# Optimization experiments

Hardware: AMD Instinct MI355X
Metric: run time of the kernel (lower is better)

## Reference

```python
import jax, jax.numpy as jnp
import numpy as np

N = 100_000      # nodes
E = 1_600_000    # edges (avg degree 16)
IN, H, OUT = 960, 192, 3
NB = 6           # block_num


def setup_inputs() -> dict:
    key = jax.random.key(0)
    ks = jax.random.split(key, 14)
    s = 0.05  # weight init scale
    x = jax.random.normal(ks[0], (N, IN), jnp.float32)
    src = jax.random.randint(ks[1], (E,), 0, N, jnp.int32)
    dst = jax.random.randint(ks[2], (E,), 0, N, jnp.int32)
    # normalized adjacency values (like D^-1 A entries)
    ew = jax.random.uniform(ks[3], (E,), jnp.float32) / 16.0
    w1 = jax.random.normal(ks[4], (IN, H), jnp.float32) * s
    l1 = jax.random.normal(ks[5], (IN, H), jnp.float32) * s
    b1 = jnp.zeros((H,), jnp.float32)
    wb = jax.random.normal(ks[6], (2 * NB, H, H), jnp.float32) * s
    lb = jax.random.normal(ks[7], (2 * NB, H, H), jnp.float32) * s
    bb = jnp.zeros((2 * NB, H), jnp.float32)
    w2 = jax.random.normal(ks[8], (H, OUT), jnp.float32) * s
    l2 = jax.random.normal(ks[9], (H, OUT), jnp.float32) * s
    b2 = jnp.zeros((OUT,), jnp.float32)
    return dict(x=x, src=src, dst=dst, ew=ew, w1=w1, l1=l1, b1=b1,
                wb=wb, lb=lb, bb=bb, w2=w2, l2=l2, b2=b2)


def reference(x, src, dst, ew, w1, l1, b1, wb, lb, bb, w2, l2, b2):
    def gcn(h, w, lw, b):
        # GraphConvolution: spmm(adj, h @ w) + h @ loop_w + b
        sup = h @ w                                   # [N, F_out]
        msg = sup[src] * ew[:, None]                  # gather + weight  [E, F_out]
        agg = jax.ops.segment_sum(msg, dst, num_segments=N)
        return agg + h @ lw + b

    h = gcn(x, w1, l1, b1)                            # conv1: in_dim -> hidden
    for i in range(NB):                               # GResBlocks
        a = gcn(h, wb[2 * i], lb[2 * i], bb[2 * i])
        a = gcn(a, wb[2 * i + 1], lb[2 * i + 1], bb[2 * i + 1])
        h = (h + a) * 0.5                             # residual scaling
    x_cat = h
    x_out = gcn(x_cat, w2, l2, b2)                    # conv2: hidden -> out_dim
    return (x_out, x_cat)
```

## Files before the change

kernel.cpp:

```cpp
#include <hip/hip_runtime.h>

typedef __attribute__((ext_vector_type(8))) short short8;
typedef __attribute__((ext_vector_type(4))) float f32x4;
typedef __attribute__((ext_vector_type(4))) int int4v;
typedef __attribute__((ext_vector_type(2))) unsigned int u32x2;

__device__ __forceinline__ float bf2f(unsigned short u) {
  return __uint_as_float(((unsigned)u) << 16);
}
__device__ __forceinline__ unsigned short f2bf(float f) {
  unsigned u = __float_as_uint(f);
  return (unsigned short)((u + 0x7FFFu + ((u >> 16) & 1u)) >> 16);
}

#define GLB_CAST(p) ((const __attribute__((address_space(1))) void*)(p))
#define LDS_CAST(p) ((__attribute__((address_space(3))) void*)(p))

__global__ void count_kernel(const int* __restrict__ dst, int* __restrict__ cnt, int E) {
  int e = blockIdx.x * blockDim.x + threadIdx.x;
  if (e < E) atomicAdd(&cnt[dst[e] + 1], 1);
}

__global__ __launch_bounds__(256) void scan_bsum_kernel(const int* __restrict__ cnt,
                                                        int* __restrict__ bsum, int n) {
  __shared__ int buf[256];
  int tid = threadIdx.x;
  int j0 = blockIdx.x * 1024 + tid * 4;
  int s = 0;
#pragma unroll
  for (int k = 0; k < 4; k++) {
    int j = j0 + k;
    if (j < n) s += cnt[j];
  }
  buf[tid] = s;
  __syncthreads();
  for (int off = 128; off > 0; off >>= 1) {
    if (tid < off) buf[tid] += buf[tid + off];
    __syncthreads();
  }
  if (tid == 0) bsum[blockIdx.x] = buf[0];
}

__global__ __launch_bounds__(256) void scan_small_kernel(const int* __restrict__ bsum,
                                                         int* __restrict__ boff, int nb) {
  __shared__ int buf[2][256];
  int tid = threadIdx.x;
  int C = (nb + 255) >> 8;
  int start = tid * C;
  int end = start + C; if (end > nb) end = nb;
  int s = 0;
  for (int j = start; j < end; j++) s += bsum[j];
  buf[0][tid] = s;
  __syncthreads();
  int pin = 0;
  for (int off = 1; off < 256; off <<= 1) {
    int v = buf[pin][tid];
    if (tid >= off) v += buf[pin][tid - off];
    buf[pin ^ 1][tid] = v;
    pin ^= 1;
    __syncthreads();
  }
  int run = (tid == 0) ? 0 : buf[pin][tid - 1];
  for (int j = start; j < end; j++) {
    boff[j] = run;
    run += bsum[j];
  }
}

__global__ __launch_bounds__(256) void scan_final_kernel(const int* __restrict__ cnt,
                                                         const int* __restrict__ boff,
                                                         int* __restrict__ rowptr,
                                                         int* __restrict__ cur,
                                                         int n, int nrows) {
  __shared__ int buf[2][256];
  int tid = threadIdx.x;
  int j0 = blockIdx.x * 1024 + tid * 4;
  int v[4];
  int s = 0;
#pragma unroll
  for (int k = 0; k < 4; k++) {
    int j = j0 + k;
    v[k] = (j < n) ? cnt[j] : 0;
    s += v[k];
  }
  buf[0][tid] = s;
  __syncthreads();
  int pin = 0;
  for (int off = 1; off < 256; off <<= 1) {
    int t = buf[pin][tid];
    if (tid >= off) t += buf[pin][tid - off];
    buf[pin ^ 1][tid] = t;
    pin ^= 1;
    __syncthreads();
  }
  int run = boff[blockIdx.x] + ((tid == 0) ? 0 : buf[pin][tid - 1]);
#pragma unroll
  for (int k = 0; k < 4; k++) {
    int j = j0 + k;
    if (j < n) {
      run += v[k];
      rowptr[j] = run;
      if (j < nrows) cur[j] = run;
    }
  }
}

__global__ void fill_kernel(const int* __restrict__ src, const int* __restrict__ dst,
                            const float* __restrict__ ew,
                            int* __restrict__ cur, int2* __restrict__ s_edge, int E) {
  int e = blockIdx.x * blockDim.x + threadIdx.x;
  if (e >= E) return;
  int r = dst[e];
  int pos = atomicAdd(&cur[r], 1);
  s_edge[pos] = make_int2(src[e], __float_as_int(ew[e]));
}

__global__ void prep_w_kernel(const float* __restrict__ w1,
                              const float* __restrict__ l1,
                              const float* __restrict__ wb,
                              const float* __restrict__ lb,
                              unsigned short* __restrict__ Wt1,
                              unsigned short* __restrict__ Wtb) {
  int tid = blockIdx.x * blockDim.x + threadIdx.x;
  const int n1 = 384 * 960;
  const int nb = 12 * 384 * 192;
  if (tid < n1) {
    int c = tid / 960, k = tid % 960;
    Wt1[tid] = f2bf((c < 192) ? w1[k * 192 + c] : l1[k * 192 + (c - 192)]);
  } else if (tid < n1 + nb) {
    int u = tid - n1;
    int i = u / (384 * 192);
    int r = u % (384 * 192);
    int c = r / 192, k = r % 192;
    Wtb[u] = f2bf((c < 192) ? wb[(i * 192 + k) * 192 + c]
                            : lb[(i * 192 + k) * 192 + (c - 192)]);
  }
}

__device__ __forceinline__ short8 cvt_pair(f32x4 a, f32x4 b) {
  short8 r;
  r[0] = (short)f2bf(a[0]); r[1] = (short)f2bf(a[1]);
  r[2] = (short)f2bf(a[2]); r[3] = (short)f2bf(a[3]);
  r[4] = (short)f2bf(b[0]); r[5] = (short)f2bf(b[1]);
  r[6] = (short)f2bf(b[2]); r[7] = (short)f2bf(b[3]);
  return r;
}

__global__ __launch_bounds__(512) void gemm_f32_kernel(const float* __restrict__ A,
                                                       const unsigned short* __restrict__ Wt,
                                                       unsigned short* __restrict__ out,
                                                       int nrows, int K) {
  __shared__ char lds_raw[40960];

  int tid = threadIdx.x;
  int lane = tid & 63;
  int w = tid >> 6;
  int rg = w >> 1, ch = w & 1;
  int row0blk = blockIdx.x * 256;
  int row0 = row0blk + rg * 64;
  int l15 = lane & 15, lq = lane >> 4;

  f32x4 acc[12][4];
#pragma unroll
  for (int cf = 0; cf < 12; cf++)
#pragma unroll
    for (int rf = 0; rf < 4; rf++) acc[cf][rf] = (f32x4)(0.0f);

  int tiles = K / 32;
  for (int tile = 0; tile < tiles; ++tile) {
    __syncthreads();
#pragma unroll
    for (int it = 0; it < 3; ++it) {
      int slot = it * 512 + tid;
      int q = slot / 384, c = slot - q * 384;
      const unsigned short* g = Wt + (size_t)c * K + tile * 32 + q * 8;
      __builtin_amdgcn_global_load_lds(GLB_CAST(g), LDS_CAST(lds_raw + 16384 + slot * 16), 16, 0, 0);
    }
#pragma unroll
    for (int it = 0; it < 2; ++it) {
      int slot = it * 512 + tid;
      int c = slot >> 8, row = slot & 255;
      int grow = row0blk + row;
      if (grow > nrows - 1) grow = nrows - 1;
      const float* g = A + (size_t)grow * K + tile * 32 + c * 8;
      f32x4 a0 = *reinterpret_cast<const f32x4*>(g);
      f32x4 a1 = *reinterpret_cast<const f32x4*>(g + 4);
      *reinterpret_cast<short8*>(lds_raw + slot * 16) = cvt_pair(a0, a1);
    }
    __syncthreads();

    short8 af[4];
#pragma unroll
    for (int rf = 0; rf < 4; rf++)
      af[rf] = *reinterpret_cast<const short8*>(
          lds_raw + lq * 4096 + (rg * 64 + rf * 16 + l15) * 16);
#pragma unroll
    for (int cf = 0; cf < 12; cf++) {
      const short8 bf = *reinterpret_cast<const short8*>(
          lds_raw + 16384 + (lq * 384 + ch * 192 + cf * 16 + l15) * 16);
#pragma unroll
      for (int rf = 0; rf < 4; rf++)
        acc[cf][rf] = __builtin_amdgcn_mfma_f32_16x16x32_bf16(bf, af[rf], acc[cf][rf], 0, 0, 0);
    }
  }

#pragma unroll
  for (int rf = 0; rf < 4; rf++) {
    int row = row0 + rf * 16 + l15;
    if (row >= nrows) continue;
    unsigned short* orow = out + (size_t)row * 384 + ch * 192 + lq * 4;
#pragma unroll
    for (int cf = 0; cf < 12; cf++) {
      u32x2 pv;
      pv[0] = (unsigned)f2bf(acc[cf][rf][0]) | ((unsigned)f2bf(acc[cf][rf][1]) << 16);
      pv[1] = (unsigned)f2bf(acc[cf][rf][2]) | ((unsigned)f2bf(acc[cf][rf][3]) << 16);
      *reinterpret_cast<u32x2*>(orow + cf * 16) = pv;
    }
  }
}

__global__ __launch_bounds__(512) void gemm_bf16_db_kernel(const unsigned short* __restrict__ A,
                                                           const unsigned short* __restrict__ Wt,
                                                           unsigned short* __restrict__ out,
                                                           int nrows, int K) {
  extern __shared__ char lds_db[];

  int tid = threadIdx.x;
  int lane = tid & 63;
  int w = tid >> 6;
  int rg = w >> 1, ch = w & 1;
  int row0blk = blockIdx.x * 256;
  int row0 = row0blk + rg * 64;
  int l15 = lane & 15, lq = lane >> 4;

  f32x4 acc[12][4];
#pragma unroll
  for (int cf = 0; cf < 12; cf++)
#pragma unroll
    for (int rf = 0; rf < 4; rf++) acc[cf][rf] = (f32x4)(0.0f);

  auto stage = [&](int tile, int buf) {
    char* base = lds_db + buf * 40960;
#pragma unroll
    for (int it = 0; it < 3; ++it) {
      int slot = it * 512 + tid;
      int q = slot / 384, c = slot - q * 384;
      const unsigned short* g = Wt + (size_t)c * K + tile * 32 + q * 8;
      __builtin_amdgcn_global_load_lds(GLB_CAST(g), LDS_CAST(base + 16384 + slot * 16), 16, 0, 0);
    }
#pragma unroll
    for (int it = 0; it < 2; ++it) {
      int slot = it * 512 + tid;
      int c = slot >> 8, row = slot & 255;
      int grow = row0blk + row;
      if (grow > nrows - 1) grow = nrows - 1;
      const unsigned short* g = A + (size_t)grow * K + tile * 32 + c * 8;
      __builtin_amdgcn_global_load_lds(GLB_CAST(g), LDS_CAST(base + slot * 16), 16, 0, 0);
    }
  };

  int tiles = K / 32;
  stage(0, 0);
  __syncthreads();
  int cur = 0;
  for (int tile = 0; tile < tiles; ++tile) {
    if (tile + 1 < tiles) stage(tile + 1, cur ^ 1);
    char* base = lds_db + cur * 40960;
    short8 af[4];
#pragma unroll
    for (int rf = 0; rf < 4; rf++)
      af[rf] = *reinterpret_cast<const short8*>(
          base + lq * 4096 + (rg * 64 + rf * 16 + l15) * 16);
#pragma unroll
    for (int cf = 0; cf < 12; cf++) {
      const short8 bf = *reinterpret_cast<const short8*>(
          base + 16384 + (lq * 384 + ch * 192 + cf * 16 + l15) * 16);
#pragma unroll
      for (int rf = 0; rf < 4; rf++)
        acc[cf][rf] = __builtin_amdgcn_mfma_f32_16x16x32_bf16(bf, af[rf], acc[cf][rf], 0, 0, 0);
    }
    __syncthreads();
    cur ^= 1;
  }

#pragma unroll
  for (int rf = 0; rf < 4; rf++) {
    int row = row0 + rf * 16 + l15;
    if (row >= nrows) continue;
    unsigned short* orow = out + (size_t)row * 384 + ch * 192 + lq * 4;
#pragma unroll
    for (int cf = 0; cf < 12; cf++) {
      u32x2 pv;
      pv[0] = (unsigned)f2bf(acc[cf][rf][0]) | ((unsigned)f2bf(acc[cf][rf][1]) << 16);
      pv[1] = (unsigned)f2bf(acc[cf][rf][2]) | ((unsigned)f2bf(acc[cf][rf][3]) << 16);
      *reinterpret_cast<u32x2*>(orow + cf * 16) = pv;
    }
  }
}

__global__ __launch_bounds__(256) void spmm_kernel(const unsigned short* __restrict__ t,
                                                   const int* __restrict__ rowptr,
                                                   const int2* __restrict__ s_edge,
                                                   const float* __restrict__ bias,
                                                   const unsigned short* __restrict__ hprev16,
                                                   unsigned short* __restrict__ out16,
                                                   int n, int mode) {
  int tid = blockIdx.x * blockDim.x + threadIdx.x;
  int node = tid >> 3;
  int sub = tid & 7;
  if (node >= n) return;
  int co = sub * 8;

  float acc[3][8];
#pragma unroll
  for (int q = 0; q < 3; q++)
#pragma unroll
    for (int j = 0; j < 8; j++) acc[q][j] = 0.0f;

  int e0 = rowptr[node], e1 = rowptr[node + 1];
  int ne = e1 - e0;
  int base = 0;
  for (; base + 8 <= ne; base += 8) {
    int2 rec = s_edge[e0 + base + sub];
#pragma unroll
    for (int half = 0; half < 2; half++) {
      short8 v[4][3];
      float wgt[4];
#pragma unroll
      for (int k = 0; k < 4; k++) {
        int kk = half * 4 + k;
        int sn = __shfl(rec.x, kk, 8);
        wgt[k] = __int_as_float(__shfl(rec.y, kk, 8));
        const unsigned short* row = t + (size_t)sn * 384;
#pragma unroll
        for (int q = 0; q < 3; q++)
          v[k][q] = *reinterpret_cast<const short8*>(row + q * 64 + co);
      }
#pragma unroll
      for (int k = 0; k < 4; k++)
#pragma unroll
        for (int q = 0; q < 3; q++)
#pragma unroll
          for (int j = 0; j < 8; j++)
            acc[q][j] += wgt[k] * bf2f((unsigned short)v[k][q][j]);
    }
  }
  for (; base < ne; base++) {
    int2 rec = s_edge[e0 + base];
    float wgt = __int_as_float(rec.y);
    const unsigned short* row = t + (size_t)rec.x * 384;
#pragma unroll
    for (int q = 0; q < 3; q++) {
      short8 v = *reinterpret_cast<const short8*>(row + q * 64 + co);
#pragma unroll
      for (int j = 0; j < 8; j++) acc[q][j] += wgt * bf2f((unsigned short)v[j]);
    }
  }

  const unsigned short* hlrow = t + (size_t)node * 384 + 192;
#pragma unroll
  for (int q = 0; q < 3; q++) {
    short8 hlv = *reinterpret_cast<const short8*>(hlrow + q * 64 + co);
    float r[8];
#pragma unroll
    for (int j = 0; j < 8; j++)
      r[j] = acc[q][j] + bf2f((unsigned short)hlv[j]) + bias[q * 64 + co + j];
    if (mode == 1) {
      short8 hp = *reinterpret_cast<const short8*>(&hprev16[(size_t)node * 192 + q * 64 + co]);
#pragma unroll
      for (int j = 0; j < 8; j++)
        r[j] = 0.5f * (bf2f((unsigned short)hp[j]) + r[j]);
    }
    unsigned short o16[8];
#pragma unroll
    for (int j = 0; j < 8; j++) o16[j] = f2bf(r[j]);
    *reinterpret_cast<int4v*>(&out16[(size_t)node * 192 + q * 64 + co]) =
        *reinterpret_cast<const int4v*>(o16);
  }
}

__global__ __launch_bounds__(256) void cvt_kernel(const unsigned short* __restrict__ h16,
                                                  float* __restrict__ h32, int n8) {
  int i = blockIdx.x * blockDim.x + threadIdx.x;
  if (i >= n8) return;
  short8 v = *reinterpret_cast<const short8*>(&h16[(size_t)i * 8]);
  f32x4 lo, hi;
#pragma unroll
  for (int j = 0; j < 4; j++) {
    lo[j] = bf2f((unsigned short)v[j]);
    hi[j] = bf2f((unsigned short)v[4 + j]);
  }
  *reinterpret_cast<f32x4*>(&h32[(size_t)i * 8]) = lo;
  *reinterpret_cast<f32x4*>(&h32[(size_t)i * 8 + 4]) = hi;
}

__global__ __launch_bounds__(256) void conv2a_kernel(const unsigned short* __restrict__ h,
                                                     const float* __restrict__ w2,
                                                     const float* __restrict__ l2,
                                                     const float* __restrict__ b2,
                                                     float* __restrict__ sup2,
                                                     float* __restrict__ hl2, int n) {
  int wid = (blockIdx.x * blockDim.x + threadIdx.x) >> 6;
  int lane = threadIdx.x & 63;
  if (wid >= n) return;
  float sa[3] = {0.f, 0.f, 0.f}, sl[3] = {0.f, 0.f, 0.f};
  for (int k = lane; k < 192; k += 64) {
    float hv = bf2f(h[(size_t)wid * 192 + k]);
#pragma unroll
    for (int j = 0; j < 3; j++) {
      sa[j] += hv * w2[k * 3 + j];
      sl[j] += hv * l2[k * 3 + j];
    }
  }
#pragma unroll
  for (int j = 0; j < 3; j++) {
    for (int off = 32; off > 0; off >>= 1) {
      sa[j] += __shfl_down(sa[j], off);
      sl[j] += __shfl_down(sl[j], off);
    }
  }
  if (lane == 0) {
#pragma unroll
    for (int j = 0; j < 3; j++) {
      sup2[(size_t)wid * 3 + j] = sa[j];
      hl2[(size_t)wid * 3 + j] = sl[j] + b2[j];
    }
  }
}

__global__ __launch_bounds__(256) void conv2b_kernel(const int* __restrict__ rowptr,
                                                     const int2* __restrict__ s_edge,
                                                     const float* __restrict__ sup2,
                                                     const float* __restrict__ hl2,
                                                     float* __restrict__ out, int n) {
  int node = blockIdx.x * blockDim.x + threadIdx.x;
  if (node >= n) return;
  float acc[3] = {0.f, 0.f, 0.f};
  int e0 = rowptr[node], e1 = rowptr[node + 1];
  for (int e = e0; e < e1; e++) {
    int2 rec = s_edge[e];
    float wgt = __int_as_float(rec.y);
#pragma unroll
    for (int j = 0; j < 3; j++) acc[j] += wgt * sup2[(size_t)rec.x * 3 + j];
  }
#pragma unroll
  for (int j = 0; j < 3; j++)
    out[(size_t)node * 3 + j] = acc[j] + hl2[(size_t)node * 3 + j];
}

extern "C" void kernel_launch(void* const* d_in, const int* in_sizes, int n_in,
                              void* d_out, int out_size, void* d_ws, size_t ws_size,
                              hipStream_t stream) {
  const float* x  = (const float*)d_in[0];
  const int* src  = (const int*)d_in[1];
  const int* dst  = (const int*)d_in[2];
  const float* ew = (const float*)d_in[3];
  const float* w1 = (const float*)d_in[4];
  const float* l1 = (const float*)d_in[5];
  const float* b1 = (const float*)d_in[6];
  const float* wb = (const float*)d_in[7];
  const float* lb = (const float*)d_in[8];
  const float* bb = (const float*)d_in[9];
  const float* w2 = (const float*)d_in[10];
  const float* l2 = (const float*)d_in[11];
  const float* b2 = (const float*)d_in[12];
  float* out = (float*)d_out;

  const int N = in_sizes[0] / 960;
  const int E = in_sizes[1];

  float* h32 = out + (size_t)N * 3;

  char* p = (char*)d_ws;
  auto alloc = [&](size_t bytes) {
    char* q = p;
    p += (bytes + 255) & ~(size_t)255;
    return q;
  };
  unsigned short* Wt1 = (unsigned short*)alloc((size_t)384 * 960 * 2);
  unsigned short* Wtb = (unsigned short*)alloc((size_t)12 * 384 * 192 * 2);
  unsigned short* t   = (unsigned short*)alloc((size_t)N * 384 * 2);
  unsigned short* h16 = (unsigned short*)alloc((size_t)N * 192 * 2);
  unsigned short* a16 = (unsigned short*)alloc((size_t)N * 192 * 2);
  int* rowptr = (int*)alloc((size_t)(N + 1) * 4);
  int* cur    = (int*)alloc((size_t)N * 4);
  int* cnt    = (int*)alloc((size_t)(N + 1) * 4);
  int* bsum   = (int*)alloc((size_t)1024 * 4);
  int* boff   = (int*)alloc((size_t)1024 * 4);
  int2* s_edge = (int2*)alloc((size_t)E * 8);
  float* sup2 = (float*)alloc((size_t)N * 3 * 4);
  float* hl2  = (float*)alloc((size_t)N * 3 * 4);
  if ((size_t)(p - (char*)d_ws) > ws_size) return;

  const int nScan = N + 1;
  const int nBlk = (nScan + 1023) / 1024;

  hipMemsetAsync(cnt, 0, (size_t)(N + 1) * 4, stream);
  count_kernel<<<(E + 255) / 256, 256, 0, stream>>>(dst, cnt, E);
  scan_bsum_kernel<<<nBlk, 256, 0, stream>>>(cnt, bsum, nScan);
  scan_small_kernel<<<1, 256, 0, stream>>>(bsum, boff, nBlk);
  scan_final_kernel<<<nBlk, 256, 0, stream>>>(cnt, boff, rowptr, cur, nScan, N);
  fill_kernel<<<(E + 255) / 256, 256, 0, stream>>>(src, dst, ew, cur, s_edge, E);
  {
    int total = 384 * 960 + 12 * 384 * 192;
    prep_w_kernel<<<(total + 255) / 256, 256, 0, stream>>>(w1, l1, wb, lb, Wt1, Wtb);
  }

  int gBlocks = (N + 255) / 256;
  int sBlocks = (N * 8 + 255) / 256;
  const int DB_LDS = 81920;

  gemm_f32_kernel<<<gBlocks, 512, 0, stream>>>(x, Wt1, t, N, 960);
  spmm_kernel<<<sBlocks, 256, 0, stream>>>(t, rowptr, s_edge, b1,
                                           (const unsigned short*)nullptr, h16, N, 0);

  for (int i = 0; i < 12; i += 2) {
    gemm_bf16_db_kernel<<<gBlocks, 512, DB_LDS, stream>>>(
        h16, Wtb + (size_t)i * 384 * 192, t, N, 192);
    spmm_kernel<<<sBlocks, 256, 0, stream>>>(t, rowptr, s_edge, bb + (size_t)i * 192,
                                             (const unsigned short*)nullptr, a16, N, 0);
    gemm_bf16_db_kernel<<<gBlocks, 512, DB_LDS, stream>>>(
        a16, Wtb + (size_t)(i + 1) * 384 * 192, t, N, 192);
    spmm_kernel<<<sBlocks, 256, 0, stream>>>(t, rowptr, s_edge, bb + (size_t)(i + 1) * 192,
                                             h16, h16, N, 1);
  }

  cvt_kernel<<<(N * 24 + 255) / 256, 256, 0, stream>>>(h16, h32, N * 24);

  conv2a_kernel<<<(N + 3) / 4, 256, 0, stream>>>(h16, w2, l2, b2, sup2, hl2, N);
  conv2b_kernel<<<(N + 255) / 256, 256, 0, stream>>>(rowptr, s_edge, sup2, hl2, out, N);
}
```

Measured before the change: 2.469 ms.

## Reorder block GCN to aggregate-then-transform with concatenated K=384 GEMM

For the residual blocks, the sparse aggregation is now applied to the 192-wide input h first (A·h), then a single GEMM over [A·h | h] with stacked [W; L] (K=384, N=192) produces the output, with bias and the residual average fused into the GEMM epilogue. This replaces a GEMM writing a 384-wide intermediate plus an SpMM reading it, so the SpMM gathers only 192-wide rows and the intermediate write is halved. The GEMM loses double buffering (single-buffered LDS, 256 threads) and the re-association changes bf16 rounding points.

```diff
diff --git a/kernel.cpp b/kernel.cpp
--- a/kernel.cpp
+++ b/kernel.cpp
@@ -120,20 +120,20 @@
                               const float* __restrict__ wb,
                               const float* __restrict__ lb,
                               unsigned short* __restrict__ Wt1,
-                              unsigned short* __restrict__ Wtb) {
+                              unsigned short* __restrict__ Wcatb) {
   int tid = blockIdx.x * blockDim.x + threadIdx.x;
   const int n1 = 384 * 960;
-  const int nb = 12 * 384 * 192;
+  const int nc = 12 * 192 * 384;
   if (tid < n1) {
     int c = tid / 960, k = tid % 960;
     Wt1[tid] = f2bf((c < 192) ? w1[k * 192 + c] : l1[k * 192 + (c - 192)]);
-  } else if (tid < n1 + nb) {
+  } else if (tid < n1 + nc) {
     int u = tid - n1;
-    int i = u / (384 * 192);
-    int r = u % (384 * 192);
-    int c = r / 192, k = r % 192;
-    Wtb[u] = f2bf((c < 192) ? wb[(i * 192 + k) * 192 + c]
-                            : lb[(i * 192 + k) * 192 + (c - 192)]);
+    int i = u / (192 * 384);
+    int r = u % (192 * 384);
+    int c = r / 384, k = r % 384;
+    Wcatb[u] = f2bf((k < 192) ? wb[((size_t)i * 192 + k) * 192 + c]
+                              : lb[((size_t)i * 192 + (k - 192)) * 192 + c]);
   }
 }
 
@@ -219,18 +219,19 @@
   }
 }
 
-__global__ __launch_bounds__(512) void gemm_bf16_db_kernel(const unsigned short* __restrict__ A,
-                                                           const unsigned short* __restrict__ Wt,
-                                                           unsigned short* __restrict__ out,
-                                                           int nrows, int K) {
-  extern __shared__ char lds_db[];
+__global__ __launch_bounds__(256) void gemm_cat_kernel(const unsigned short* __restrict__ A1,
+                                                       const unsigned short* __restrict__ A2,
+                                                       const unsigned short* __restrict__ Wcat,
+                                                       const float* __restrict__ bias,
+                                                       const unsigned short* __restrict__ hprev,
+                                                       unsigned short* __restrict__ out,
+                                                       int nrows) {
+  __shared__ char lds[28672];
 
   int tid = threadIdx.x;
   int lane = tid & 63;
-  int w = tid >> 6;
-  int rg = w >> 1, ch = w & 1;
+  int rg = tid >> 6;
   int row0blk = blockIdx.x * 256;
-  int row0 = row0blk + rg * 64;
   int l15 = lane & 15, lq = lane >> 4;
 
   f32x4 acc[12][4];
@@ -239,72 +240,78 @@
 #pragma unroll
     for (int rf = 0; rf < 4; rf++) acc[cf][rf] = (f32x4)(0.0f);
 
-  auto stage = [&](int tile, int buf) {
-    char* base = lds_db + buf * 40960;
+  for (int tile = 0; tile < 12; ++tile) {
+    __syncthreads();
 #pragma unroll
     for (int it = 0; it < 3; ++it) {
-      int slot = it * 512 + tid;
-      int q = slot / 384, c = slot - q * 384;
-      const unsigned short* g = Wt + (size_t)c * K + tile * 32 + q * 8;
-      __builtin_amdgcn_global_load_lds(GLB_CAST(g), LDS_CAST(base + 16384 + slot * 16), 16, 0, 0);
-    }
-#pragma unroll
-    for (int it = 0; it < 2; ++it) {
-      int slot = it * 512 + tid;
-      int c = slot >> 8, row = slot & 255;
-      int grow = row0blk + row;
-      if (grow > nrows - 1) grow = nrows - 1;
-      const unsigned short* g = A + (size_t)grow * K + tile * 32 + c * 8;
-      __builtin_amdgcn_global_load_lds(GLB_CAST(g), LDS_CAST(base + slot * 16), 16, 0, 0);
-    }
-  };
-
-  int tiles = K / 32;
-  stage(0, 0);
-  __syncthreads();
-  int cur = 0;
-  for (int tile = 0; tile < tiles; ++tile) {
-    if (tile + 1 < tiles) stage(tile + 1, cur ^ 1);
-    char* base = lds_db + cur * 40960;
+      int slot = it * 256 + tid;
+      int q = slot / 192, c = slot - q * 192;
+      const unsigned short* g = Wcat + (size_t)c * 384 + tile * 32 + q * 8;
+      __builtin_amdgcn_global_load_lds(GLB_CAST(g), LDS_CAST(lds + 16384 + slot * 16), 16, 0, 0);
+    }
+    {
+      const unsigned short* arr = (tile < 6) ? A1 : A2;
+      int koff = (tile < 6 ? tile : tile - 6) * 32;
+#pragma unroll
+      for (int it = 0; it < 4; ++it) {
+        int slot = it * 256 + tid;
+        int q = slot >> 8, row = slot & 255;
+        int grow = row0blk + row;
+        if (grow > nrows - 1) grow = nrows - 1;
+        const unsigned short* g = arr + (size_t)grow * 192 + koff + q * 8;
+        __builtin_amdgcn_global_load_lds(GLB_CAST(g), LDS_CAST(lds + slot * 16), 16, 0, 0);
+      }
+    }
+    __syncthreads();
+
     short8 af[4];
 #pragma unroll
     for (int rf = 0; rf < 4; rf++)
       af[rf] = *reinterpret_cast<const short8*>(
-          base + lq * 4096 + (rg * 64 + rf * 16 + l15) * 16);
+          lds + (lq * 256 + rg * 64 + rf * 16 + l15) * 16);
 #pragma unroll
     for (int cf = 0; cf < 12; cf++) {
       const short8 bf = *reinterpret_cast<const short8*>(
-          base + 16384 + (lq * 384 + ch * 192 + cf * 16 + l15) * 16);
+          lds + 16384 + (lq * 192 + cf * 16 + l15) * 16);
 #pragma unroll
       for (int rf = 0; rf < 4; rf++)
         acc[cf][rf] = __builtin_amdgcn_mfma_f32_16x16x32_bf16(bf, af[rf], acc[cf][rf], 0, 0, 0);
     }
-    __syncthreads();
-    cur ^= 1;
   }
 
 #pragma unroll
   for (int rf = 0; rf < 4; rf++) {
-    int row = row0 + rf * 16 + l15;
+    int row = row0blk + rg * 64 + rf * 16 + l15;
     if (row >= nrows) continue;
-    unsigned short* orow = out + (size_t)row * 384 + ch * 192 + lq * 4;
+    unsigned short* orow = out + (size_t)row * 192 + lq * 4;
 #pragma unroll
     for (int cf = 0; cf < 12; cf++) {
+      int col = cf * 16 + lq * 4;
+      f32x4 bv = *reinterpret_cast<const f32x4*>(bias + col);
+      float r[4];
+#pragma unroll
+      for (int j = 0; j < 4; j++) r[j] = acc[cf][rf][j] + bv[j];
+      if (hprev) {
+        u32x2 hp = *reinterpret_cast<const u32x2*>(&hprev[(size_t)row * 192 + col]);
+        r[0] = 0.5f * (bf2f((unsigned short)(hp[0] & 0xFFFF)) + r[0]);
+        r[1] = 0.5f * (bf2f((unsigned short)(hp[0] >> 16)) + r[1]);
+        r[2] = 0.5f * (bf2f((unsigned short)(hp[1] & 0xFFFF)) + r[2]);
+        r[3] = 0.5f * (bf2f((unsigned short)(hp[1] >> 16)) + r[3]);
+      }
       u32x2 pv;
-      pv[0] = (unsigned)f2bf(acc[cf][rf][0]) | ((unsigned)f2bf(acc[cf][rf][1]) << 16);
-      pv[1] = (unsigned)f2bf(acc[cf][rf][2]) | ((unsigned)f2bf(acc[cf][rf][3]) << 16);
+      pv[0] = (unsigned)f2bf(r[0]) | ((unsigned)f2bf(r[1]) << 16);
+      pv[1] = (unsigned)f2bf(r[2]) | ((unsigned)f2bf(r[3]) << 16);
       *reinterpret_cast<u32x2*>(orow + cf * 16) = pv;
     }
   }
 }
 
-__global__ __launch_bounds__(256) void spmm_kernel(const unsigned short* __restrict__ t,
-                                                   const int* __restrict__ rowptr,
-                                                   const int2* __restrict__ s_edge,
-                                                   const float* __restrict__ bias,
-                                                   const unsigned short* __restrict__ hprev16,
-                                                   unsigned short* __restrict__ out16,
-                                                   int n, int mode) {
+__global__ __launch_bounds__(256) void spmm_t_kernel(const unsigned short* __restrict__ t,
+                                                     const int* __restrict__ rowptr,
+                                                     const int2* __restrict__ s_edge,
+                                                     const float* __restrict__ bias,
+                                                     unsigned short* __restrict__ out16,
+                                                     int n) {
   int tid = blockIdx.x * blockDim.x + threadIdx.x;
   int node = tid >> 3;
   int sub = tid & 7;
@@ -361,20 +368,78 @@
 #pragma unroll
   for (int q = 0; q < 3; q++) {
     short8 hlv = *reinterpret_cast<const short8*>(hlrow + q * 64 + co);
-    float r[8];
+    unsigned short o16[8];
 #pragma unroll
     for (int j = 0; j < 8; j++)
-      r[j] = acc[q][j] + bf2f((unsigned short)hlv[j]) + bias[q * 64 + co + j];
-    if (mode == 1) {
-      short8 hp = *reinterpret_cast<const short8*>(&hprev16[(size_t)node * 192 + q * 64 + co]);
-#pragma unroll
-      for (int j = 0; j < 8; j++)
-        r[j] = 0.5f * (bf2f((unsigned short)hp[j]) + r[j]);
-    }
+      o16[j] = f2bf(acc[q][j] + bf2f((unsigned short)hlv[j]) + bias[q * 64 + co + j]);
+    *reinterpret_cast<int4v*>(&out16[(size_t)node * 192 + q * 64 + co]) =
+        *reinterpret_cast<const int4v*>(o16);
+  }
+}
+
+__global__ __launch_bounds__(256) void spmm_g_kernel(const unsigned short* __restrict__ h,
+                                                     const int* __restrict__ rowptr,
+                                                     const int2* __restrict__ s_edge,
+                                                     unsigned short* __restrict__ g16,
+                                                     int n) {
+  int tid = blockIdx.x * blockDim.x + threadIdx.x;
+  int node = tid >> 3;
+  int sub = tid & 7;
+  if (node >= n) return;
+  int co = sub * 8;
+
+  float acc[3][8];
+#pragma unroll
+  for (int q = 0; q < 3; q++)
+#pragma unroll
+    for (int j = 0; j < 8; j++) acc[q][j] = 0.0f;
+
+  int e0 = rowptr[node], e1 = rowptr[node + 1];
+  int ne = e1 - e0;
+  int base = 0;
+  for (; base + 8 <= ne; base += 8) {
+    int2 rec = s_edge[e0 + base + sub];
+#pragma unroll
+    for (int half = 0; half < 2; half++) {
+      short8 v[4][3];
+      float wgt[4];
+#pragma unroll
+      for (int k = 0; k < 4; k++) {
+        int kk = half * 4 + k;
+        int sn = __shfl(rec.x, kk, 8);
+        wgt[k] = __int_as_float(__shfl(rec.y, kk, 8));
+        const unsigned short* row = h + (size_t)sn * 192;
+#pragma unroll
+        for (int q = 0; q < 3; q++)
+          v[k][q] = *reinterpret_cast<const short8*>(row + q * 64 + co);
+      }
+#pragma unroll
+      for (int k = 0; k < 4; k++)
+#pragma unroll
+        for (int q = 0; q < 3; q++)
+#pragma unroll
+          for (int j = 0; j < 8; j++)
+            acc[q][j] += wgt[k] * bf2f((unsigned short)v[k][q][j]);
+    }
+  }
+  for (; base < ne; base++) {
+    int2 rec = s_edge[e0 + base];
+    float wgt = __int_as_float(rec.y);
+    const unsigned short* row = h + (size_t)rec.x * 192;
+#pragma unroll
+    for (int q = 0; q < 3; q++) {
+      short8 v = *reinterpret_cast<const short8*>(row + q * 64 + co);
+#pragma unroll
+      for (int j = 0; j < 8; j++) acc[q][j] += wgt * bf2f((unsigned short)v[j]);
+    }
+  }
+
+#pragma unroll
+  for (int q = 0; q < 3; q++) {
     unsigned short o16[8];
 #pragma unroll
-    for (int j = 0; j < 8; j++) o16[j] = f2bf(r[j]);
-    *reinterpret_cast<int4v*>(&out16[(size_t)node * 192 + q * 64 + co]) =
+    for (int j = 0; j < 8; j++) o16[j] = f2bf(acc[q][j]);
+    *reinterpret_cast<int4v*>(&g16[(size_t)node * 192 + q * 64 + co]) =
         *reinterpret_cast<const int4v*>(o16);
   }
 }
@@ -477,11 +542,11 @@
     p += (bytes + 255) & ~(size_t)255;
     return q;
   };
-  unsigned short* Wt1 = (unsigned short*)alloc((size_t)384 * 960 * 2);
-  unsigned short* Wtb = (unsigned short*)alloc((size_t)12 * 384 * 192 * 2);
-  unsigned short* t   = (unsigned short*)alloc((size_t)N * 384 * 2);
-  unsigned short* h16 = (unsigned short*)alloc((size_t)N * 192 * 2);
-  unsigned short* a16 = (unsigned short*)alloc((size_t)N * 192 * 2);
+  unsigned short* Wt1   = (unsigned short*)alloc((size_t)384 * 960 * 2);
+  unsigned short* Wcatb = (unsigned short*)alloc((size_t)12 * 192 * 384 * 2);
+  unsigned short* t     = (unsigned short*)alloc((size_t)N * 384 * 2);
+  unsigned short* h16a  = (unsigned short*)alloc((size_t)N * 192 * 2);
+  unsigned short* h16b  = (unsigned short*)alloc((size_t)N * 192 * 2);
   int* rowptr = (int*)alloc((size_t)(N + 1) * 4);
   int* cur    = (int*)alloc((size_t)N * 4);
   int* cnt    = (int*)alloc((size_t)(N + 1) * 4);
@@ -492,6 +557,9 @@
   float* hl2  = (float*)alloc((size_t)N * 3 * 4);
   if ((size_t)(p - (char*)d_ws) > ws_size) return;
 
+  unsigned short* g16 = t;
+  unsigned short* a16 = t + (size_t)N * 192;
+
   const int nScan = N + 1;
   const int nBlk = (nScan + 1023) / 1024;
 
@@ -502,31 +570,32 @@
   scan_final_kernel<<<nBlk, 256, 0, stream>>>(cnt, boff, rowptr, cur, nScan, N);
   fill_kernel<<<(E + 255) / 256, 256, 0, stream>>>(src, dst, ew, cur, s_edge, E);
   {
-    int total = 384 * 960 + 12 * 384 * 192;
-    prep_w_kernel<<<(total + 255) / 256, 256, 0, stream>>>(w1, l1, wb, lb, Wt1, Wtb);
+    int total = 384 * 960 + 12 * 192 * 384;
+    prep_w_kernel<<<(total + 255) / 256, 256, 0, stream>>>(w1, l1, wb, lb, Wt1, Wcatb);
   }
 
   int gBlocks = (N + 255) / 256;
   int sBlocks = (N * 8 + 255) / 256;
-  const int DB_LDS = 81920;
 
   gemm_f32_kernel<<<gBlocks, 512, 0, stream>>>(x, Wt1, t, N, 960);
-  spmm_kernel<<<sBlocks, 256, 0, stream>>>(t, rowptr, s_edge, b1,
-                                           (const unsigned short*)nullptr, h16, N, 0);
-
+  spmm_t_kernel<<<sBlocks, 256, 0, stream>>>(t, rowptr, s_edge, b1, h16a, N);
+
+  unsigned short* hcur = h16a;
+  unsigned short* hnxt = h16b;
   for (int i = 0; i < 12; i += 2) {
-    gemm_bf16_db_kernel<<<gBlocks, 512, DB_LDS, stream>>>(
-        h16, Wtb + (size_t)i * 384 * 192, t, N, 192);
-    spmm_kernel<<<sBlocks, 256, 0, stream>>>(t, rowptr, s_edge, bb + (size_t)i * 192,
-                                             (const unsigned short*)nullptr, a16, N, 0);
-    gemm_bf16_db_kernel<<<gBlocks, 512, DB_LDS, stream>>>(
-        a16, Wtb + (size_t)(i + 1) * 384 * 192, t, N, 192);
-    spmm_kernel<<<sBlocks, 256, 0, stream>>>(t, rowptr, s_edge, bb + (size_t)(i + 1) * 192,
-                                             h16, h16, N, 1);
-  }
-
-  cvt_kernel<<<(N * 24 + 255) / 256, 256, 0, stream>>>(h16, h32, N * 24);
-
-  conv2a_kernel<<<(N + 3) / 4, 256, 0, stream>>>(h16, w2, l2, b2, sup2, hl2, N);
+    spmm_g_kernel<<<sBlocks, 256, 0, stream>>>(hcur, rowptr, s_edge, g16, N);
+    gemm_cat_kernel<<<gBlocks, 256, 0, stream>>>(
+        g16, hcur, Wcatb + (size_t)i * 192 * 384, bb + (size_t)i * 192,
+        (const unsigned short*)nullptr, a16, N);
+    spmm_g_kernel<<<sBlocks, 256, 0, stream>>>(a16, rowptr, s_edge, g16, N);
+    gemm_cat_kernel<<<gBlocks, 256, 0, stream>>>(
+        g16, a16, Wcatb + (size_t)(i + 1) * 192 * 384, bb + (size_t)(i + 1) * 192,
+        hcur, hnxt, N);
+    unsigned short* tmp = hcur; hcur = hnxt; hnxt = tmp;
+  }
+
+  cvt_kernel<<<(N * 24 + 255) / 256, 256, 0, stream>>>(hcur, h32, N * 24);
+
+  conv2a_kernel<<<(N + 3) / 4, 256, 0, stream>>>(hcur, w2, l2, b2, sup2, hl2, N);
   conv2b_kernel<<<(N + 255) / 256, 256, 0, stream>>>(rowptr, s_edge, sup2, hl2, out, N);
 }
```

Measured after the change: 2.653 ms. +7.5%, slower.
